# Performance work log

Measured on AMD Instinct MI355X. Metric: run time of the kernel, lower is better.

The kernel has to match this reference:

```python
import jax, jax.numpy as jnp
import numpy as np

EMBED_DIM = 512
NUM_HEADS = 8
N_WIRES = 8  # kernel uses only first N_WIRES dims of each head vector


def setup_inputs() -> dict:
    key = jax.random.key(0)
    x = jax.random.normal(key, (8, 1024, EMBED_DIM), dtype=jnp.float32)
    return {"x": x}


def reference(x):
    B, S, E = x.shape
    H = NUM_HEADS
    dk = E // H
    # [B, H, S, dk]
    xh = x.reshape(B, S, H, dk).transpose(0, 2, 1, 3)
    # Quantum RY-overlap kernel closed form:
    #   RY(-y) RY(x) |0> = RY(x - y) |0>  =>  <0...0|psi> = prod_w cos((x_w - y_w)/2)
    # Only the first N_WIRES components of each head vector are used
    # (states.view(-1)[0] reads the first batch row's |0..0> amplitude).
    xw = xh[..., :N_WIRES]  # [B, H, S, NW]
    scores = jnp.ones((B, H, S, S), dtype=x.dtype)
    for w in range(N_WIRES):  # fixed small loop, fuses under jit
        diff = xw[:, :, :, None, w] - xw[:, :, None, :, w]  # [B, H, S, S]
        scores = scores * jnp.cos(diff * 0.5)
    scores = jnp.abs(scores)
    attn = jax.nn.softmax(scores, axis=-1)  # dropout is identity at eval
    out = jnp.einsum("bhij,bhjd->bhid", attn, xh)  # [B, H, S, dk]
    return out.transpose(0, 2, 1, 3).reshape(B, S, E)
```

## Files before the change

### kernel.cpp

```cpp
#include <hip/hip_runtime.h>

#define B_  8
#define S_  1024
#define E_  512
#define TI  64
#define TJ  64
#define LOG2E 1.44269504088896340736f

typedef _Float16 half_t;
typedef _Float16 half2_t __attribute__((ext_vector_type(2)));
typedef _Float16 half8_t __attribute__((ext_vector_type(8)));
typedef float    floatx16 __attribute__((ext_vector_type(16)));
typedef unsigned int uint2v __attribute__((ext_vector_type(2)));
typedef unsigned int uint4v __attribute__((ext_vector_type(4)));

#define PHI_BYTES ((size_t)64 * S_ * 32 * 2)
#define VT_BYTES  ((size_t)64 * 16 * 4096 * 2)

#define GLOAD_LDS16(g, l)                                                        \
    __builtin_amdgcn_global_load_lds((const __attribute__((address_space(1))) void*)(g), \
                                     (__attribute__((address_space(3))) void*)(l), 16, 0, 0)

__global__ __launch_bounds__(256, 4) void precompute_kernel(const float* __restrict__ x,
                                                            half_t* __restrict__ phiA,
                                                            half_t* __restrict__ phiB,
                                                            half_t* __restrict__ vt) {
    const int orig = blockIdx.x;
    const int xcd  = orig & 7, slot = orig >> 3;
    const int bh   = xcd * 8 + (slot & 7);
    const int chunk = slot >> 3;
    const int b  = bh >> 3, h = bh & 7;
    const int j0 = chunk * 64;
    const int t  = threadIdx.x;
    __shared__ __align__(16) float vf[64][76];

    const float* xb = x + (size_t)b * S_ * E_ + h * 64;

    {
        const int j = t >> 2, dq = (t & 3) * 4;
        const float* row = xb + (size_t)(j0 + j) * E_;
        #pragma unroll
        for (int q = 0; q < 4; ++q)
            *(float4*)&vf[j][dq + q * 16] = *(const float4*)(row + dq + q * 16);
    }
    __syncthreads();

    if (t < 128) {
        const int jj = t >> 1, sel = t & 1;
        float4 xw = *(const float4*)&vf[jj][sel * 4];
        float xi[4] = {xw.x, xw.y, xw.z, xw.w};
        float c[4], s[4];
        #pragma unroll
        for (int q = 0; q < 4; ++q) {
            float v = xi[q] * 0.5f;
            c[q] = __cosf(v); s[q] = __sinf(v);
        }
        float pa[4] = {c[0]*c[1], s[0]*c[1], c[0]*s[1], s[0]*s[1]};
        float pb[4] = {c[2]*c[3], s[2]*c[3], c[2]*s[3], s[2]*s[3]};
        const float scale = sel ? LOG2E : 1.0f;
        half_t hB[16], hA[16];
        #pragma unroll
        for (int f = 0; f < 16; ++f) {
            float v = pa[f & 3] * pb[f >> 2];
            hB[f] = (half_t)v;
            hA[f] = (half_t)(v * scale);
        }
        size_t off = ((size_t)bh * S_ + j0 + jj) * 32 + (sel ? 0 : 16);
        *(half8_t*)(phiB + off)     = *(half8_t*)&hB[0];
        *(half8_t*)(phiB + off + 8) = *(half8_t*)&hB[8];
        *(half8_t*)(phiA + off)     = *(half8_t*)&hA[0];
        *(half8_t*)(phiA + off + 8) = *(half8_t*)&hA[8];
    }

    {
        const int d = t >> 2, jg = (t & 3) * 16;
        half_t hv[16];
        #pragma unroll
        for (int k = 0; k < 16; ++k) hv[k] = (half_t)vf[jg + k][d];
        const int slot0 = (t & 3) * 2;
        half_t* base = vt + ((size_t)bh * 16 + chunk) * 4096;
        *(half8_t*)(base + (slot0 + 0) * 512 + d * 8) = *(half8_t*)&hv[0];
        *(half8_t*)(base + (slot0 + 1) * 512 + d * 8) = *(half8_t*)&hv[8];
    }
}

__global__ __launch_bounds__(256, 2) void attn_kernel(const half_t* __restrict__ phiA,
                                                      const half_t* __restrict__ phiB,
                                                      const half_t* __restrict__ vt,
                                                      float* __restrict__ out) {
    const int orig = blockIdx.x;
    const int xcd  = orig & 7, slot = orig >> 3;
    const int bh   = xcd * 8 + (slot & 7);
    const int iblk = slot >> 3;
    const int b    = bh >> 3, h = bh & 7;
    const int i0   = iblk * TI;
    const int t    = threadIdx.x;
    const int wv   = t >> 6, ln = t & 63;
    const int m    = ln & 31, hf = ln >> 5;
    const int ib   = wv >> 1, jb = wv & 1;

    __shared__ __align__(16) unsigned char smem_u[16384];
    half_t (&sh_v)[2][4096]     = *reinterpret_cast<half_t(*)[2][4096]>(smem_u);
    float  (&sh_red)[2][32][64] = *reinterpret_cast<float(*)[2][32][64]>(smem_u);
    __shared__ float sh_den[2][64];

    const half_t* phbA = phiA + (size_t)bh * S_ * 32;
    const half_t* phbB = phiB + (size_t)bh * S_ * 32;
    const half_t* vtb  = vt + (size_t)bh * 16 * 4096;

    half8_t biH, biL;
    {
        const half_t* pr = phbB + (size_t)(i0 + ib * 32 + m) * 32 + hf * 8;
        biH = *(const half8_t*)pr;
        biL = *(const half8_t*)(pr + 16);
    }

    floatx16 acc0, acc1, z;
    #pragma unroll
    for (int k = 0; k < 16; ++k) { acc0[k] = 0.f; acc1[k] = 0.f; z[k] = 0.f; }
    float d0 = 0.f, d1 = 0.f;

    const half_t* asrc = phbA + (size_t)(jb * 32 + m) * 32 + hf * 8;
    const int s0 = 2 * wv, s1 = 2 * wv + 1;

    GLOAD_LDS16(vtb + s0 * 512 + ln * 8, &sh_v[0][s0 * 512]);
    GLOAD_LDS16(vtb + s1 * 512 + ln * 8, &sh_v[0][s1 * 512]);
    __builtin_amdgcn_sched_barrier(0);
    half8_t ajH = *(const half8_t*)(asrc);
    half8_t ajL = *(const half8_t*)(asrc + 16);
    asm volatile("s_waitcnt vmcnt(2)" ::: "memory");
    __builtin_amdgcn_s_barrier();

    #pragma unroll 2
    for (int tt = 0; tt < 16; ++tt) {
        const int cur = tt & 1;
        const int ntt = (tt + 1) & 15;

        if (tt < 15) {
            const half_t* vs = vtb + (size_t)ntt * 4096;
            GLOAD_LDS16(vs + s0 * 512 + ln * 8, &sh_v[cur ^ 1][s0 * 512]);
            GLOAD_LDS16(vs + s1 * 512 + ln * 8, &sh_v[cur ^ 1][s1 * 512]);
        }
        __builtin_amdgcn_sched_barrier(0);

        const half_t* vb = sh_v[cur];
        const int q0 = jb * 4;
        half8_t b00 = *(const half8_t*)&vb[(q0 + 0 + hf) * 512 + m * 8];
        half8_t b01 = *(const half8_t*)&vb[(q0 + 2 + hf) * 512 + m * 8];
        half8_t b10 = *(const half8_t*)&vb[(q0 + 0 + hf) * 512 + (32 + m) * 8];
        half8_t b11 = *(const half8_t*)&vb[(q0 + 2 + hf) * 512 + (32 + m) * 8];

        const half_t* ar = asrc + (size_t)(ntt * TJ) * 32;
        half8_t ajHn = *(const half8_t*)ar;
        half8_t ajLn = *(const half8_t*)(ar + 16);

        floatx16 sH = __builtin_amdgcn_mfma_f32_32x32x16_f16(ajH, biH, z, 0, 0, 0);
        floatx16 sL = __builtin_amdgcn_mfma_f32_32x32x16_f16(ajL, biL, z, 0, 0, 0);

        unsigned int dwa[4], dwb[4];
        #pragma unroll
        for (int g = 0; g < 4; ++g) {
            float p[4];
            #pragma unroll
            for (int r = 0; r < 4; ++r) {
                float sc = sH[4 * g + r] * sL[4 * g + r];
                p[r] = __builtin_amdgcn_exp2f(__builtin_fabsf(sc));
            }
            d0 += p[0] + p[2];
            d1 += p[1] + p[3];
            half2_t ha = {(half_t)p[0], (half_t)p[1]};
            half2_t hb = {(half_t)p[2], (half_t)p[3]};
            dwa[g] = __builtin_bit_cast(unsigned int, ha);
            dwb[g] = __builtin_bit_cast(unsigned int, hb);
        }
        uint2v swA0 = __builtin_amdgcn_permlane32_swap(dwa[0], dwa[1], false, false);
        uint2v swB0 = __builtin_amdgcn_permlane32_swap(dwb[0], dwb[1], false, false);
        uint2v swA1 = __builtin_amdgcn_permlane32_swap(dwa[2], dwa[3], false, false);
        uint2v swB1 = __builtin_amdgcn_permlane32_swap(dwb[2], dwb[3], false, false);
        half8_t ap0 = __builtin_bit_cast(half8_t, (uint4v){swA0.x, swB0.x, swA0.y, swB0.y});
        half8_t ap1 = __builtin_bit_cast(half8_t, (uint4v){swA1.x, swB1.x, swA1.y, swB1.y});

        acc0 = __builtin_amdgcn_mfma_f32_32x32x16_f16(ap0, b00, acc0, 0, 0, 0);
        acc0 = __builtin_amdgcn_mfma_f32_32x32x16_f16(ap1, b01, acc0, 0, 0, 0);
        acc1 = __builtin_amdgcn_mfma_f32_32x32x16_f16(ap0, b10, acc1, 0, 0, 0);
        acc1 = __builtin_amdgcn_mfma_f32_32x32x16_f16(ap1, b11, acc1, 0, 0, 0);

        if (tt < 15) { asm volatile("s_waitcnt vmcnt(2)" ::: "memory"); }
        __builtin_amdgcn_s_barrier();
        ajH = ajHn; ajL = ajLn;
    }

    __syncthreads();

    float dtot = d0 + d1;
    dtot += __shfl_xor(dtot, 32, 64);
    sh_den[jb][ib * 32 + m] = dtot;
    if (jb == 1) {
        #pragma unroll
        for (int reg = 0; reg < 16; ++reg) {
            int il = (reg & 3) + 8 * (reg >> 2) + 4 * hf;
            sh_red[ib][il][m]      = acc0[reg];
            sh_red[ib][il][32 + m] = acc1[reg];
        }
    }
    __syncthreads();
    if (jb == 0) {
        #pragma unroll
        for (int reg = 0; reg < 16; ++reg) {
            int il = (reg & 3) + 8 * (reg >> 2) + 4 * hf;
            float inv = 1.f / (sh_den[0][ib * 32 + il] + sh_den[1][ib * 32 + il]);
            size_t base = ((size_t)(b * S_ + i0 + ib * 32 + il)) * E_ + h * 64 + m;
            __builtin_nontemporal_store((acc0[reg] + sh_red[ib][il][m])      * inv, &out[base]);
            __builtin_nontemporal_store((acc1[reg] + sh_red[ib][il][32 + m]) * inv, &out[base + 32]);
        }
    }
}

extern "C" void kernel_launch(void* const* d_in, const int* in_sizes, int n_in,
                              void* d_out, int out_size, void* d_ws, size_t ws_size,
                              hipStream_t stream) {
    const float* x = (const float*)d_in[0];
    float* out = (float*)d_out;
    half_t* phiA = (half_t*)d_ws;
    half_t* phiB = (half_t*)((char*)d_ws + PHI_BYTES);
    half_t* vt   = (half_t*)((char*)d_ws + 2 * PHI_BYTES);
    precompute_kernel<<<dim3(1024), 256, 0, stream>>>(x, phiA, phiB, vt);
    attn_kernel<<<dim3(1024), 256, 0, stream>>>(phiA, phiB, vt, out);
}
```

Measured before the change: 93.05 us.

## Process 256-key j-tiles per iteration with four sub-blocks per wave

The attention loop now steps over 256 keys per stage instead of 64, so there are 4 stages instead of 16. Each wave handles four 32-key sub-blocks per stage, and V tiles are staged as 32KB double buffers in 64KB of LDS. The goal is to cut per-iteration barrier and wait overhead and give the MFMA and exp work more independent instructions to interleave. In exchange, the LDS footprint and register pressure rise sharply, which may lower occupancy below the two-block launch bound.

Result: slower. 95.62 us (+2.8%).

```diff
diff --git a/kernel.cpp b/kernel.cpp
--- a/kernel.cpp
+++ b/kernel.cpp
@@ -3,8 +3,6 @@
 #define B_  8
 #define S_  1024
 #define E_  512
-#define TI  64
-#define TJ  64
 #define LOG2E 1.44269504088896340736f
 
 typedef _Float16 half_t;
@@ -93,20 +91,20 @@
     const int bh   = xcd * 8 + (slot & 7);
     const int iblk = slot >> 3;
     const int b    = bh >> 3, h = bh & 7;
-    const int i0   = iblk * TI;
+    const int i0   = iblk * 64;
     const int t    = threadIdx.x;
     const int wv   = t >> 6, ln = t & 63;
     const int m    = ln & 31, hf = ln >> 5;
     const int ib   = wv >> 1, jb = wv & 1;
 
-    __shared__ __align__(16) unsigned char smem_u[16384];
-    half_t (&sh_v)[2][4096]     = *reinterpret_cast<half_t(*)[2][4096]>(smem_u);
+    __shared__ __align__(16) unsigned char smem_u[65536];
+    half_t (&sh_v)[2][16384]    = *reinterpret_cast<half_t(*)[2][16384]>(smem_u);
     float  (&sh_red)[2][32][64] = *reinterpret_cast<float(*)[2][32][64]>(smem_u);
-    __shared__ float sh_den[2][64];
+    float  (&sh_den)[2][64]     = *reinterpret_cast<float(*)[2][64]>(smem_u + 16384 * 4);
 
     const half_t* phbA = phiA + (size_t)bh * S_ * 32;
     const half_t* phbB = phiB + (size_t)bh * S_ * 32;
-    const half_t* vtb  = vt + (size_t)bh * 16 * 4096;
+    const half_t* vtb  = vt + (size_t)bh * 65536;
 
     half8_t biH, biL;
     {
@@ -120,74 +118,88 @@
     for (int k = 0; k < 16; ++k) { acc0[k] = 0.f; acc1[k] = 0.f; z[k] = 0.f; }
     float d0 = 0.f, d1 = 0.f;
 
-    const half_t* asrc = phbA + (size_t)(jb * 32 + m) * 32 + hf * 8;
-    const int s0 = 2 * wv, s1 = 2 * wv + 1;
-
-    GLOAD_LDS16(vtb + s0 * 512 + ln * 8, &sh_v[0][s0 * 512]);
-    GLOAD_LDS16(vtb + s1 * 512 + ln * 8, &sh_v[0][s1 * 512]);
+    const int s0 = 8 * wv;
+
+    #pragma unroll
+    for (int i = 0; i < 8; ++i)
+        GLOAD_LDS16(vtb + (s0 + i) * 512 + ln * 8, &sh_v[0][(s0 + i) * 512]);
     __builtin_amdgcn_sched_barrier(0);
-    half8_t ajH = *(const half8_t*)(asrc);
-    half8_t ajL = *(const half8_t*)(asrc + 16);
-    asm volatile("s_waitcnt vmcnt(2)" ::: "memory");
+    half8_t aH[4], aL[4];
+    #pragma unroll
+    for (int qi = 0; qi < 4; ++qi) {
+        const half_t* ar = phbA + (size_t)((jb + 2 * qi) * 32 + m) * 32 + hf * 8;
+        aH[qi] = *(const half8_t*)ar;
+        aL[qi] = *(const half8_t*)(ar + 16);
+    }
+    asm volatile("s_waitcnt vmcnt(8)" ::: "memory");
     __builtin_amdgcn_s_barrier();
 
-    #pragma unroll 2
-    for (int tt = 0; tt < 16; ++tt) {
+    #pragma unroll
+    for (int tt = 0; tt < 4; ++tt) {
         const int cur = tt & 1;
-        const int ntt = (tt + 1) & 15;
-
-        if (tt < 15) {
-            const half_t* vs = vtb + (size_t)ntt * 4096;
-            GLOAD_LDS16(vs + s0 * 512 + ln * 8, &sh_v[cur ^ 1][s0 * 512]);
-            GLOAD_LDS16(vs + s1 * 512 + ln * 8, &sh_v[cur ^ 1][s1 * 512]);
+        const int np  = (tt + 1) & 3;
+
+        if (tt < 3) {
+            const half_t* vs = vtb + (size_t)(tt + 1) * 16384;
+            #pragma unroll
+            for (int i = 0; i < 8; ++i)
+                GLOAD_LDS16(vs + (s0 + i) * 512 + ln * 8, &sh_v[cur ^ 1][(s0 + i) * 512]);
         }
         __builtin_amdgcn_sched_barrier(0);
 
-        const half_t* vb = sh_v[cur];
-        const int q0 = jb * 4;
-        half8_t b00 = *(const half8_t*)&vb[(q0 + 0 + hf) * 512 + m * 8];
-        half8_t b01 = *(const half8_t*)&vb[(q0 + 2 + hf) * 512 + m * 8];
-        half8_t b10 = *(const half8_t*)&vb[(q0 + 0 + hf) * 512 + (32 + m) * 8];
-        half8_t b11 = *(const half8_t*)&vb[(q0 + 2 + hf) * 512 + (32 + m) * 8];
-
-        const half_t* ar = asrc + (size_t)(ntt * TJ) * 32;
-        half8_t ajHn = *(const half8_t*)ar;
-        half8_t ajLn = *(const half8_t*)(ar + 16);
-
-        floatx16 sH = __builtin_amdgcn_mfma_f32_32x32x16_f16(ajH, biH, z, 0, 0, 0);
-        floatx16 sL = __builtin_amdgcn_mfma_f32_32x32x16_f16(ajL, biL, z, 0, 0, 0);
-
-        unsigned int dwa[4], dwb[4];
-        #pragma unroll
-        for (int g = 0; g < 4; ++g) {
-            float p[4];
+        half8_t nH[4], nL[4];
+        #pragma unroll
+        for (int qi = 0; qi < 4; ++qi) {
+            const half_t* ar = phbA + (size_t)(np * 256 + (jb + 2 * qi) * 32 + m) * 32 + hf * 8;
+            nH[qi] = *(const half8_t*)ar;
+            nL[qi] = *(const half8_t*)(ar + 16);
+        }
+
+        #pragma unroll
+        for (int qi = 0; qi < 4; ++qi) {
+            const int q = jb + 2 * qi;
+            const half_t* vb = sh_v[cur];
+            half8_t b00 = *(const half8_t*)&vb[(q * 4 + 0 + hf) * 512 + m * 8];
+            half8_t b01 = *(const half8_t*)&vb[(q * 4 + 2 + hf) * 512 + m * 8];
+            half8_t b10 = *(const half8_t*)&vb[(q * 4 + 0 + hf) * 512 + (32 + m) * 8];
+            half8_t b11 = *(const half8_t*)&vb[(q * 4 + 2 + hf) * 512 + (32 + m) * 8];
+
+            floatx16 sH = __builtin_amdgcn_mfma_f32_32x32x16_f16(aH[qi], biH, z, 0, 0, 0);
+            floatx16 sL = __builtin_amdgcn_mfma_f32_32x32x16_f16(aL[qi], biL, z, 0, 0, 0);
+
+            unsigned int dwa[4], dwb[4];
             #pragma unroll
-            for (int r = 0; r < 4; ++r) {
-                float sc = sH[4 * g + r] * sL[4 * g + r];
-                p[r] = __builtin_amdgcn_exp2f(__builtin_fabsf(sc));
+            for (int g = 0; g < 4; ++g) {
+                float p[4];
+                #pragma unroll
+                for (int r = 0; r < 4; ++r) {
+                    float sc = sH[4 * g + r] * sL[4 * g + r];
+                    p[r] = __builtin_amdgcn_exp2f(__builtin_fabsf(sc));
+                }
+                d0 += p[0] + p[2];
+                d1 += p[1] + p[3];
+                half2_t ha = {(half_t)p[0], (half_t)p[1]};
+                half2_t hb = {(half_t)p[2], (half_t)p[3]};
+                dwa[g] = __builtin_bit_cast(unsigned int, ha);
+                dwb[g] = __builtin_bit_cast(unsigned int, hb);
             }
-            d0 += p[0] + p[2];
-            d1 += p[1] + p[3];
-            half2_t ha = {(half_t)p[0], (half_t)p[1]};
-            half2_t hb = {(half_t)p[2], (half_t)p[3]};
-            dwa[g] = __builtin_bit_cast(unsigned int, ha);
-            dwb[g] = __builtin_bit_cast(unsigned int, hb);
-        }
-        uint2v swA0 = __builtin_amdgcn_permlane32_swap(dwa[0], dwa[1], false, false);
-        uint2v swB0 = __builtin_amdgcn_permlane32_swap(dwb[0], dwb[1], false, false);
-        uint2v swA1 = __builtin_amdgcn_permlane32_swap(dwa[2], dwa[3], false, false);
-        uint2v swB1 = __builtin_amdgcn_permlane32_swap(dwb[2], dwb[3], false, false);
-        half8_t ap0 = __builtin_bit_cast(half8_t, (uint4v){swA0.x, swB0.x, swA0.y, swB0.y});
-        half8_t ap1 = __builtin_bit_cast(half8_t, (uint4v){swA1.x, swB1.x, swA1.y, swB1.y});
-
-        acc0 = __builtin_amdgcn_mfma_f32_32x32x16_f16(ap0, b00, acc0, 0, 0, 0);
-        acc0 = __builtin_amdgcn_mfma_f32_32x32x16_f16(ap1, b01, acc0, 0, 0, 0);
-        acc1 = __builtin_amdgcn_mfma_f32_32x32x16_f16(ap0, b10, acc1, 0, 0, 0);
-        acc1 = __builtin_amdgcn_mfma_f32_32x32x16_f16(ap1, b11, acc1, 0, 0, 0);
-
-        if (tt < 15) { asm volatile("s_waitcnt vmcnt(2)" ::: "memory"); }
+            uint2v swA0 = __builtin_amdgcn_permlane32_swap(dwa[0], dwa[1], false, false);
+            uint2v swB0 = __builtin_amdgcn_permlane32_swap(dwb[0], dwb[1], false, false);
+            uint2v swA1 = __builtin_amdgcn_permlane32_swap(dwa[2], dwa[3], false, false);
+            uint2v swB1 = __builtin_amdgcn_permlane32_swap(dwb[2], dwb[3], false, false);
+            half8_t ap0 = __builtin_bit_cast(half8_t, (uint4v){swA0.x, swB0.x, swA0.y, swB0.y});
+            half8_t ap1 = __builtin_bit_cast(half8_t, (uint4v){swA1.x, swB1.x, swA1.y, swB1.y});
+
+            acc0 = __builtin_amdgcn_mfma_f32_32x32x16_f16(ap0, b00, acc0, 0, 0, 0);
+            acc0 = __builtin_amdgcn_mfma_f32_32x32x16_f16(ap1, b01, acc0, 0, 0, 0);
+            acc1 = __builtin_amdgcn_mfma_f32_32x32x16_f16(ap0, b10, acc1, 0, 0, 0);
+            acc1 = __builtin_amdgcn_mfma_f32_32x32x16_f16(ap1, b11, acc1, 0, 0, 0);
+        }
+
+        if (tt < 3) { asm volatile("s_waitcnt vmcnt(8)" ::: "memory"); }
         __builtin_amdgcn_s_barrier();
-        ajH = ajHn; ajL = ajLn;
+        #pragma unroll
+        for (int qi = 0; qi < 4; ++qi) { aH[qi] = nH[qi]; aL[qi] = nL[qi]; }
     }
 
     __syncthreads();
```

## Load V operands directly from global memory, dropping LDS double buffering and barriers

Applied to the files above, without the earlier changes.

The attention kernel no longer stages V tiles into shared memory with async global-to-LDS loads and per-iteration barriers. Each wave now reads its V fragments and phiA rows straight from global memory in a restructured loop (4 outer steps × 4 unrolled sub-tiles). This removes the block-wide barrier and waitcnt synchronisation on every tile. In exchange, V is fetched redundantly by the waves that share it, and explicit prefetch overlap is lost, so latency hiding now depends on the compiler's scheduling and the caches.

Result: slower. 105.4 us (+13.3%).

```diff
diff --git a/kernel.cpp b/kernel.cpp
--- a/kernel.cpp
+++ b/kernel.cpp
@@ -3,8 +3,6 @@
 #define B_  8
 #define S_  1024
 #define E_  512
-#define TI  64
-#define TJ  64
 #define LOG2E 1.44269504088896340736f
 
 typedef _Float16 half_t;
@@ -16,10 +14,6 @@
 
 #define PHI_BYTES ((size_t)64 * S_ * 32 * 2)
 #define VT_BYTES  ((size_t)64 * 16 * 4096 * 2)
-
-#define GLOAD_LDS16(g, l)                                                        \
-    __builtin_amdgcn_global_load_lds((const __attribute__((address_space(1))) void*)(g), \
-                                     (__attribute__((address_space(3))) void*)(l), 16, 0, 0)
 
 __global__ __launch_bounds__(256, 4) void precompute_kernel(const float* __restrict__ x,
                                                             half_t* __restrict__ phiA,
@@ -93,20 +87,18 @@
     const int bh   = xcd * 8 + (slot & 7);
     const int iblk = slot >> 3;
     const int b    = bh >> 3, h = bh & 7;
-    const int i0   = iblk * TI;
+    const int i0   = iblk * 64;
     const int t    = threadIdx.x;
     const int wv   = t >> 6, ln = t & 63;
     const int m    = ln & 31, hf = ln >> 5;
     const int ib   = wv >> 1, jb = wv & 1;
 
-    __shared__ __align__(16) unsigned char smem_u[16384];
-    half_t (&sh_v)[2][4096]     = *reinterpret_cast<half_t(*)[2][4096]>(smem_u);
-    float  (&sh_red)[2][32][64] = *reinterpret_cast<float(*)[2][32][64]>(smem_u);
+    __shared__ float sh_red[2][32][64];
     __shared__ float sh_den[2][64];
 
     const half_t* phbA = phiA + (size_t)bh * S_ * 32;
     const half_t* phbB = phiB + (size_t)bh * S_ * 32;
-    const half_t* vtb  = vt + (size_t)bh * 16 * 4096;
+    const half_t* vtb  = vt + (size_t)bh * 65536;
 
     half8_t biH, biL;
     {
@@ -120,77 +112,53 @@
     for (int k = 0; k < 16; ++k) { acc0[k] = 0.f; acc1[k] = 0.f; z[k] = 0.f; }
     float d0 = 0.f, d1 = 0.f;
 
-    const half_t* asrc = phbA + (size_t)(jb * 32 + m) * 32 + hf * 8;
-    const int s0 = 2 * wv, s1 = 2 * wv + 1;
+    for (int tt = 0; tt < 4; ++tt) {
+        const half_t* vbase = vtb + (size_t)tt * 16384;
+        #pragma unroll
+        for (int qi = 0; qi < 4; ++qi) {
+            const int q = jb + 2 * qi;
 
-    GLOAD_LDS16(vtb + s0 * 512 + ln * 8, &sh_v[0][s0 * 512]);
-    GLOAD_LDS16(vtb + s1 * 512 + ln * 8, &sh_v[0][s1 * 512]);
-    __builtin_amdgcn_sched_barrier(0);
-    half8_t ajH = *(const half8_t*)(asrc);
-    half8_t ajL = *(const half8_t*)(asrc + 16);
-    asm volatile("s_waitcnt vmcnt(2)" ::: "memory");
-    __builtin_amdgcn_s_barrier();
+            half8_t b00 = *(const half8_t*)&vbase[(q * 4 + 0 + hf) * 512 + m * 8];
+            half8_t b01 = *(const half8_t*)&vbase[(q * 4 + 2 + hf) * 512 + m * 8];
+            half8_t b10 = *(const half8_t*)&vbase[(q * 4 + 0 + hf) * 512 + (32 + m) * 8];
+            half8_t b11 = *(const half8_t*)&vbase[(q * 4 + 2 + hf) * 512 + (32 + m) * 8];
 
-    #pragma unroll 2
-    for (int tt = 0; tt < 16; ++tt) {
-        const int cur = tt & 1;
-        const int ntt = (tt + 1) & 15;
+            const half_t* ar = phbA + (size_t)(tt * 256 + q * 32 + m) * 32 + hf * 8;
+            half8_t ajH = *(const half8_t*)ar;
+            half8_t ajL = *(const half8_t*)(ar + 16);
 
-        if (tt < 15) {
-            const half_t* vs = vtb + (size_t)ntt * 4096;
-            GLOAD_LDS16(vs + s0 * 512 + ln * 8, &sh_v[cur ^ 1][s0 * 512]);
-            GLOAD_LDS16(vs + s1 * 512 + ln * 8, &sh_v[cur ^ 1][s1 * 512]);
+            floatx16 sH = __builtin_amdgcn_mfma_f32_32x32x16_f16(ajH, biH, z, 0, 0, 0);
+            floatx16 sL = __builtin_amdgcn_mfma_f32_32x32x16_f16(ajL, biL, z, 0, 0, 0);
+
+            unsigned int dwa[4], dwb[4];
+            #pragma unroll
+            for (int g = 0; g < 4; ++g) {
+                float p[4];
+                #pragma unroll
+                for (int r = 0; r < 4; ++r) {
+                    float sc = sH[4 * g + r] * sL[4 * g + r];
+                    p[r] = __builtin_amdgcn_exp2f(__builtin_fabsf(sc));
+                }
+                d0 += p[0] + p[2];
+                d1 += p[1] + p[3];
+                half2_t ha = {(half_t)p[0], (half_t)p[1]};
+                half2_t hb = {(half_t)p[2], (half_t)p[3]};
+                dwa[g] = __builtin_bit_cast(unsigned int, ha);
+                dwb[g] = __builtin_bit_cast(unsigned int, hb);
+            }
+            uint2v swA0 = __builtin_amdgcn_permlane32_swap(dwa[0], dwa[1], false, false);
+            uint2v swB0 = __builtin_amdgcn_permlane32_swap(dwb[0], dwb[1], false, false);
+            uint2v swA1 = __builtin_amdgcn_permlane32_swap(dwa[2], dwa[3], false, false);
+            uint2v swB1 = __builtin_amdgcn_permlane32_swap(dwb[2], dwb[3], false, false);
+            half8_t ap0 = __builtin_bit_cast(half8_t, (uint4v){swA0.x, swB0.x, swA0.y, swB0.y});
+            half8_t ap1 = __builtin_bit_cast(half8_t, (uint4v){swA1.x, swB1.x, swA1.y, swB1.y});
+
+            acc0 = __builtin_amdgcn_mfma_f32_32x32x16_f16(ap0, b00, acc0, 0, 0, 0);
+            acc0 = __builtin_amdgcn_mfma_f32_32x32x16_f16(ap1, b01, acc0, 0, 0, 0);
+            acc1 = __builtin_amdgcn_mfma_f32_32x32x16_f16(ap0, b10, acc1, 0, 0, 0);
+            acc1 = __builtin_amdgcn_mfma_f32_32x32x16_f16(ap1, b11, acc1, 0, 0, 0);
         }
-        __builtin_amdgcn_sched_barrier(0);
-
-        const half_t* vb = sh_v[cur];
-        const int q0 = jb * 4;
-        half8_t b00 = *(const half8_t*)&vb[(q0 + 0 + hf) * 512 + m * 8];
-        half8_t b01 = *(const half8_t*)&vb[(q0 + 2 + hf) * 512 + m * 8];
-        half8_t b10 = *(const half8_t*)&vb[(q0 + 0 + hf) * 512 + (32 + m) * 8];
-        half8_t b11 = *(const half8_t*)&vb[(q0 + 2 + hf) * 512 + (32 + m) * 8];
-
-        const half_t* ar = asrc + (size_t)(ntt * TJ) * 32;
-        half8_t ajHn = *(const half8_t*)ar;
-        half8_t ajLn = *(const half8_t*)(ar + 16);
-
-        floatx16 sH = __builtin_amdgcn_mfma_f32_32x32x16_f16(ajH, biH, z, 0, 0, 0);
-        floatx16 sL = __builtin_amdgcn_mfma_f32_32x32x16_f16(ajL, biL, z, 0, 0, 0);
-
-        unsigned int dwa[4], dwb[4];
-        #pragma unroll
-        for (int g = 0; g < 4; ++g) {
-            float p[4];
-            #pragma unroll
-            for (int r = 0; r < 4; ++r) {
-                float sc = sH[4 * g + r] * sL[4 * g + r];
-                p[r] = __builtin_amdgcn_exp2f(__builtin_fabsf(sc));
-            }
-            d0 += p[0] + p[2];
-            d1 += p[1] + p[3];
-            half2_t ha = {(half_t)p[0], (half_t)p[1]};
-            half2_t hb = {(half_t)p[2], (half_t)p[3]};
-            dwa[g] = __builtin_bit_cast(unsigned int, ha);
-            dwb[g] = __builtin_bit_cast(unsigned int, hb);
-        }
-        uint2v swA0 = __builtin_amdgcn_permlane32_swap(dwa[0], dwa[1], false, false);
-        uint2v swB0 = __builtin_amdgcn_permlane32_swap(dwb[0], dwb[1], false, false);
-        uint2v swA1 = __builtin_amdgcn_permlane32_swap(dwa[2], dwa[3], false, false);
-        uint2v swB1 = __builtin_amdgcn_permlane32_swap(dwb[2], dwb[3], false, false);
-        half8_t ap0 = __builtin_bit_cast(half8_t, (uint4v){swA0.x, swB0.x, swA0.y, swB0.y});
-        half8_t ap1 = __builtin_bit_cast(half8_t, (uint4v){swA1.x, swB1.x, swA1.y, swB1.y});
-
-        acc0 = __builtin_amdgcn_mfma_f32_32x32x16_f16(ap0, b00, acc0, 0, 0, 0);
-        acc0 = __builtin_amdgcn_mfma_f32_32x32x16_f16(ap1, b01, acc0, 0, 0, 0);
-        acc1 = __builtin_amdgcn_mfma_f32_32x32x16_f16(ap0, b10, acc1, 0, 0, 0);
-        acc1 = __builtin_amdgcn_mfma_f32_32x32x16_f16(ap1, b11, acc1, 0, 0, 0);
-
-        if (tt < 15) { asm volatile("s_waitcnt vmcnt(2)" ::: "memory"); }
-        __builtin_amdgcn_s_barrier();
-        ajH = ajHn; ajL = ajLn;
     }
-
-    __syncthreads();
 
     float dtot = d0 + d1;
     dtot += __shfl_xor(dtot, 32, 64);
```
